# Kernel optimization log

Measured on AMD Instinct MI355X. Metric: run time of the kernel, lower is better.

## Reference

```python
import jax, jax.numpy as jnp
import numpy as np

N_NODES = 50000
N_EDGES = 800000
N_REL = 6
N_LAYERS = 8
D = 256
NUM_GRAPHS = 512


def setup_inputs() -> dict:
    key = jax.random.key(0)
    ks = jax.random.split(key, 24)
    s = lambda *sh: 1.0 / np.sqrt(sh[0])
    inp = {
        "x": jax.random.normal(ks[0], (N_NODES, 13), dtype=jnp.float32),
        "edge_index": jax.random.randint(ks[1], (2, N_EDGES), 0, N_NODES, dtype=jnp.int64),
        "edge_type": jax.random.randint(ks[2], (N_EDGES,), 0, N_REL, dtype=jnp.int64),
        "batch": jnp.sort(jax.random.randint(ks[3], (N_NODES,), 0, NUM_GRAPHS, dtype=jnp.int64)),
        "enc_W": jax.random.normal(ks[4], (13, D), dtype=jnp.float32) * s(13),
        "enc_b": jnp.zeros((D,), dtype=jnp.float32),
        "prelu_a": jnp.float32(0.25),
        "rel_W": jax.random.normal(ks[5], (N_LAYERS, N_REL, D, D), dtype=jnp.float32) * s(D),
        "root_W": jax.random.normal(ks[6], (N_LAYERS, D, D), dtype=jnp.float32) * s(D),
        "conv_b": jnp.zeros((N_LAYERS, D), dtype=jnp.float32),
        "gp_W1": jax.random.normal(ks[7], (D, D), dtype=jnp.float32) * s(D),
        "gp_b1": jnp.zeros((D,), dtype=jnp.float32),
        "gp_W2": jax.random.normal(ks[8], (D, D), dtype=jnp.float32) * s(D),
        "gp_b2": jnp.zeros((D,), dtype=jnp.float32),
        "fc_W1": jax.random.normal(ks[9], (D, 1024), dtype=jnp.float32) * s(D),
        "fc_b1": jnp.zeros((1024,), dtype=jnp.float32),
        "fc_W2": jax.random.normal(ks[10], (1024, 512), dtype=jnp.float32) * s(1024),
        "fc_b2": jnp.zeros((512,), dtype=jnp.float32),
        "out_W": jax.random.normal(ks[11], (512, 1), dtype=jnp.float32) * s(512),
        "out_b": jnp.zeros((1,), dtype=jnp.float32),
    }
    return inp


def reference(x, edge_index, edge_type, batch, enc_W, enc_b, prelu_a, rel_W, root_W,
              conv_b, gp_W1, gp_b1, gp_W2, gp_b2, fc_W1, fc_b1, fc_W2, fc_b2, out_W, out_b):
    src, dst = edge_index[0], edge_index[1]
    h = x @ enc_W + enc_b  # [N, D]
    for i in range(N_LAYERS):
        skip = h
        # per-relation transform for all nodes: [R, N, D]
        xW = jnp.einsum('nd,rde->rne', h, rel_W[i])
        msgs = xW[edge_type, src]  # [E, D] gather by (relation, source node)
        agg = jax.ops.segment_sum(msgs, dst, num_segments=N_NODES)
        h = agg + h @ root_W[i] + conv_b[i]
        h = h + skip
        h = jnp.where(h > 0, h, prelu_a * h)  # PReLU (shared scalar)
        norm = jnp.sqrt(jnp.sum(h * h, axis=1, keepdims=True))
        h = h / jnp.maximum(norm, 1e-12)  # F.normalize(p=2, dim=1)
    g = jax.nn.relu(h @ gp_W1 + gp_b1) @ gp_W2 + gp_b2
    pooled = jax.ops.segment_sum(g, batch, num_segments=NUM_GRAPHS)  # global_add_pool
    z = jax.nn.relu(pooled @ fc_W1 + fc_b1)  # dropout = identity at eval
    z = jax.nn.relu(z @ fc_W2 + fc_b2)
    return jax.nn.relu(z @ out_W + out_b)  # [NUM_GRAPHS, 1]
```

## Files before the change

### kernel.cpp

```cpp
#include <hip/hip_runtime.h>

#define N_NODES   50000
#define N_EDGES   800000
#define N_REL     6
#define N_LAYERS  8
#define DD        256
#define NUM_GRAPHS 512

#define NKEYS      (N_REL * N_NODES)
#define SCAN_T     256
#define SCAN_E     8
#define SCAN_CHUNK (SCAN_T * SCAN_E)
#define SCAN_NB    ((NKEYS + SCAN_CHUNK - 1) / SCAN_CHUNK)

typedef _Float16 h4 __attribute__((ext_vector_type(4)));
typedef _Float16 h8 __attribute__((ext_vector_type(8)));
typedef float    f4 __attribute__((ext_vector_type(4)));

__device__ __forceinline__ void atomAddF(float* p, float v) { unsafeAtomicAdd(p, v); }

__device__ __forceinline__ void load_lds16(const void* g, void* l) {
    __builtin_amdgcn_global_load_lds(
        (const __attribute__((address_space(1))) uint32_t*)g,
        (__attribute__((address_space(3))) uint32_t*)l, 16, 0, 0);
}

__global__ __launch_bounds__(256) void enc_kernel(const float* __restrict__ x,
                                                  const float* __restrict__ W,
                                                  const float* __restrict__ b,
                                                  _Float16* __restrict__ Hhi,
                                                  _Float16* __restrict__ Hlo) {
    int n = blockIdx.x;
    int d = threadIdx.x;
    float s = b[d];
#pragma unroll
    for (int k = 0; k < 13; ++k) s = fmaf(x[n * 13 + k], W[k * 256 + d], s);
    const _Float16 hi = (_Float16)s;
    Hhi[(size_t)n * DD + d] = hi;
    Hlo[(size_t)n * DD + d] = (_Float16)(s - (float)hi);
}

__global__ __launch_bounds__(256) void wsplit_rel_kernel(const float* __restrict__ relW,
                                                         const float* __restrict__ rootW,
                                                         _Float16* __restrict__ wthi,
                                                         _Float16* __restrict__ wtlo) {
    const size_t id = (size_t)blockIdx.x * 256 + threadIdx.x;
    if (id >= (size_t)N_LAYERS * 7 * 256 * 256) return;
    const int k = (int)(id & 255);
    const int n = (int)((id >> 8) & 255);
    const int g = (int)((id >> 16) % 7);
    const int L = (int)((id >> 16) / 7);
    float w = (g < 6)
        ? relW[(((size_t)L * 6 + g) * 256 + k) * 256 + n]
        : rootW[((size_t)L * 256 + k) * 256 + n];
    if (g == 6 && k == n) w += 1.0f;
    const _Float16 hi = (_Float16)w;
    const size_t o = ((size_t)L * 256 + n) * 1792 + (size_t)g * 256 + k;
    wthi[o] = hi;
    wtlo[o] = (_Float16)(w - (float)hi);
}

__global__ __launch_bounds__(256) void wsplit_tr_kernel(const float* __restrict__ W,
                                                        _Float16* __restrict__ whi,
                                                        _Float16* __restrict__ wlo,
                                                        int K, int N) {
    const size_t id = (size_t)blockIdx.x * 256 + threadIdx.x;
    if (id >= (size_t)K * N) return;
    const int k = (int)(id % K), n = (int)(id / K);
    const float w = W[(size_t)k * N + n];
    const _Float16 hi = (_Float16)w;
    whi[(size_t)n * K + k] = hi;
    wlo[(size_t)n * K + k] = (_Float16)(w - (float)hi);
}

__global__ __launch_bounds__(256) void fsplit_kernel(const float* __restrict__ S,
                                                     _Float16* __restrict__ hi,
                                                     _Float16* __restrict__ lo, int total) {
    const int id = blockIdx.x * 256 + threadIdx.x;
    if (id >= total) return;
    const float v = S[id];
    const _Float16 h = (_Float16)v;
    hi[id] = h;
    lo[id] = (_Float16)(v - (float)h);
}

template <int MODE>
__global__ __launch_bounds__(256, 2) void gemm_lds(
    const _Float16* __restrict__ Ahi, const _Float16* __restrict__ Alo,
    const _Float16* __restrict__ Hhi, const _Float16* __restrict__ Hlo,
    const _Float16* __restrict__ Bhi, const _Float16* __restrict__ Blo,
    int lda, int ldb, int ldc, int boff_agg, int boff_h, int K_agg, int K_tot,
    float* __restrict__ Cf, _Float16* __restrict__ Ohi, _Float16* __restrict__ Olo,
    const float* __restrict__ bias, const float* __restrict__ pa,
    float* __restrict__ ss4, int M) {
    __shared__ _Float16 smem[16384];
    const int lane = threadIdx.x & 63;
    const int wave = threadIdx.x >> 6;
    const int lm = lane & 15, lq = lane >> 4;
    const int wm = wave & 1, wn = wave >> 1;
    const int mb = blockIdx.x * 128;
    const int nb = blockIdx.y * 128;

    int uoff[2], arowg[2], browg[2], achk[2];
#pragma unroll
    for (int q = 0; q < 2; ++q) {
        const int u    = (q * 4 + wave) * 64 + lane;
        const int row  = u >> 2;
        const int slot = u & 3;
        const int c    = slot ^ ((row >> 1) & 3);
        uoff[q] = (q * 4 + wave) * 64;
        int rg = mb + row; if (rg >= M) rg = M - 1;
        arowg[q] = rg;
        browg[q] = nb + row;
        achk[q]  = c * 8;
    }

    f4 acc[4][4];
#pragma unroll
    for (int i = 0; i < 4; ++i)
#pragma unroll
        for (int j = 0; j < 4; ++j) acc[i][j] = (f4){0.f, 0.f, 0.f, 0.f};

    for (int k0 = 0; k0 < K_tot; k0 += 32) {
        const _Float16 *pAh, *pAl;
        int acol, bcol;
        if (k0 < K_agg) {
            const size_t pb = (size_t)(k0 >> 8) * (size_t)N_NODES * DD;
            pAh = Ahi + pb; pAl = Alo + pb;
            acol = k0 & 255;
            bcol = boff_agg + k0;
        } else {
            pAh = Hhi; pAl = Hlo;
            acol = k0 - K_agg;
            bcol = boff_h + (k0 - K_agg);
        }

        __syncthreads();
#pragma unroll
        for (int q = 0; q < 2; ++q) {
            const size_t ga = (size_t)arowg[q] * lda + acol + achk[q];
            const size_t gb = (size_t)browg[q] * ldb + bcol + achk[q];
            _Float16* lbase = smem + (size_t)uoff[q] * 8;
            load_lds16(pAh + ga, lbase);
            load_lds16(pAl + ga, lbase + 4096);
            load_lds16(Bhi + gb, lbase + 8192);
            load_lds16(Blo + gb, lbase + 12288);
        }
        __syncthreads();

        h8 ah[4], al[4], bh[4], bl[4];
#pragma unroll
        for (int i = 0; i < 4; ++i) {
            const int row  = wm * 64 + i * 16 + lm;
            const int slot = lq ^ ((row >> 1) & 3);
            const int o    = (row * 4 + slot) * 8;
            ah[i] = *(const h8*)(smem + o);
            al[i] = *(const h8*)(smem + 4096 + o);
        }
#pragma unroll
        for (int j = 0; j < 4; ++j) {
            const int n    = wn * 64 + j * 16 + lm;
            const int slot = lq ^ ((n >> 1) & 3);
            const int o    = (n * 4 + slot) * 8;
            bh[j] = *(const h8*)(smem + 8192 + o);
            bl[j] = *(const h8*)(smem + 12288 + o);
        }
#pragma unroll
        for (int i = 0; i < 4; ++i)
#pragma unroll
            for (int j = 0; j < 4; ++j) {
                acc[i][j] = __builtin_amdgcn_mfma_f32_16x16x32_f16(ah[i], bh[j], acc[i][j], 0, 0, 0);
                acc[i][j] = __builtin_amdgcn_mfma_f32_16x16x32_f16(ah[i], bl[j], acc[i][j], 0, 0, 0);
                acc[i][j] = __builtin_amdgcn_mfma_f32_16x16x32_f16(al[i], bh[j], acc[i][j], 0, 0, 0);
            }
    }

    if (MODE == 0) {
#pragma unroll
        for (int i = 0; i < 4; ++i)
#pragma unroll
            for (int r = 0; r < 4; ++r) {
                const int row = mb + wm * 64 + i * 16 + lq * 4 + r;
                if (row >= M) continue;
#pragma unroll
                for (int j = 0; j < 4; ++j) {
                    const int col = nb + wn * 64 + j * 16 + lm;
                    Cf[(size_t)row * ldc + col] = acc[i][j][r] + bias[col];
                }
            }
    } else if (MODE == 3) {
#pragma unroll
        for (int i = 0; i < 4; ++i)
#pragma unroll
            for (int r = 0; r < 4; ++r) {
                const int row = mb + wm * 64 + i * 16 + lq * 4 + r;
                if (row >= M) continue;
#pragma unroll
                for (int j = 0; j < 4; ++j) {
                    const int col = nb + wn * 64 + j * 16 + lm;
                    Cf[(size_t)row * ldc + col] += acc[i][j][r];
                }
            }
    } else if (MODE == 2) {
#pragma unroll
        for (int i = 0; i < 4; ++i)
#pragma unroll
            for (int r = 0; r < 4; ++r) {
                const int row = mb + wm * 64 + i * 16 + lq * 4 + r;
                if (row >= M) continue;
#pragma unroll
                for (int j = 0; j < 4; ++j) {
                    const int col = nb + wn * 64 + j * 16 + lm;
                    const float v = fmaxf(acc[i][j][r] + bias[col], 0.f);
                    const _Float16 hi = (_Float16)v;
                    const size_t idx = (size_t)row * ldc + col;
                    Ohi[idx] = hi;
                    Olo[idx] = (_Float16)(v - (float)hi);
                }
            }
    } else {
        const float a = pa[0];
#pragma unroll
        for (int i = 0; i < 4; ++i)
#pragma unroll
            for (int r = 0; r < 4; ++r) {
                const int row = mb + wm * 64 + i * 16 + lq * 4 + r;
                float rss = 0.f;
                if (row < M) {
#pragma unroll
                    for (int j = 0; j < 4; ++j) {
                        const int col = nb + wn * 64 + j * 16 + lm;
                        float v = acc[i][j][r] + Cf[(size_t)row * ldc + col];
                        v = v > 0.f ? v : a * v;
                        const _Float16 hi = (_Float16)v;
                        const size_t idx = (size_t)row * ldc + col;
                        Ohi[idx] = hi;
                        Olo[idx] = (_Float16)(v - (float)hi);
                        rss = fmaf(v, v, rss);
                    }
                }
                rss += __shfl_xor(rss, 1, 64);
                rss += __shfl_xor(rss, 2, 64);
                rss += __shfl_xor(rss, 4, 64);
                rss += __shfl_xor(rss, 8, 64);
                if (lm == 0 && row < M)
                    ss4[(size_t)row * 4 + blockIdx.y * 2 + wn] = rss;
            }
    }
}

__global__ __launch_bounds__(256) void norm_kernel(_Float16* __restrict__ Hhi,
                                                   _Float16* __restrict__ Hlo,
                                                   const float* __restrict__ ss4) {
    const int node = blockIdx.x * 4 + (threadIdx.x >> 6);
    const int lane = threadIdx.x & 63;
    if (node >= N_NODES) return;
    const float tot = ss4[node * 4 + 0] + ss4[node * 4 + 1] +
                      ss4[node * 4 + 2] + ss4[node * 4 + 3];
    const float inv = 1.0f / fmaxf(sqrtf(tot), 1e-12f);
    const size_t o = (size_t)node * DD + lane * 4;
    h4 vh = *(const h4*)(Hhi + o);
    h4 vl = *(const h4*)(Hlo + o);
    h4 oh, ol;
#pragma unroll
    for (int e = 0; e < 4; ++e) {
        const float v = ((float)vh[e] + (float)vl[e]) * inv;
        oh[e] = (_Float16)v;
        ol[e] = (_Float16)(v - (float)oh[e]);
    }
    *(h4*)(Hhi + o) = oh;
    *(h4*)(Hlo + o) = ol;
}

__global__ __launch_bounds__(256) void hist_kernel(const int* __restrict__ dst,
                                                   const int* __restrict__ etype,
                                                   int* __restrict__ cnt) {
    const int e = blockIdx.x * 256 + threadIdx.x;
    if (e >= N_EDGES) return;
    atomicAdd(&cnt[etype[e] * N_NODES + dst[e]], 1);
}

__global__ __launch_bounds__(SCAN_T) void scan1_kernel(const int* __restrict__ cnt,
                                                       int* __restrict__ off,
                                                       int* __restrict__ bsum) {
    __shared__ int sh[SCAN_T];
    const int b = blockIdx.x, t = threadIdx.x;
    const int base = b * SCAN_CHUNK + t * SCAN_E;
    int pre[SCAN_E];
    int s = 0;
#pragma unroll
    for (int i = 0; i < SCAN_E; ++i) {
        const int x = (base + i < NKEYS) ? cnt[base + i] : 0;
        pre[i] = s;
        s += x;
    }
    sh[t] = s;
    __syncthreads();
    for (int d = 1; d < SCAN_T; d <<= 1) {
        const int x = (t >= d) ? sh[t - d] : 0;
        __syncthreads();
        sh[t] += x;
        __syncthreads();
    }
    const int toff = (t == 0) ? 0 : sh[t - 1];
#pragma unroll
    for (int i = 0; i < SCAN_E; ++i)
        if (base + i < NKEYS) off[base + i] = toff + pre[i];
    if (t == SCAN_T - 1) bsum[b] = sh[SCAN_T - 1];
}

__global__ __launch_bounds__(SCAN_T) void scan2_kernel(int* __restrict__ bsum, int n) {
    __shared__ int sh[SCAN_T];
    const int t = threadIdx.x;
    const int base = t * SCAN_E;
    int pre[SCAN_E];
    int s = 0;
#pragma unroll
    for (int i = 0; i < SCAN_E; ++i) {
        const int x = (base + i < n) ? bsum[base + i] : 0;
        pre[i] = s;
        s += x;
    }
    sh[t] = s;
    __syncthreads();
    for (int d = 1; d < SCAN_T; d <<= 1) {
        const int x = (t >= d) ? sh[t - d] : 0;
        __syncthreads();
        sh[t] += x;
        __syncthreads();
    }
    const int toff = (t == 0) ? 0 : sh[t - 1];
#pragma unroll
    for (int i = 0; i < SCAN_E; ++i)
        if (base + i < n) bsum[base + i] = toff + pre[i];
}

__global__ __launch_bounds__(SCAN_T) void scan3_kernel(int* __restrict__ off,
                                                       const int* __restrict__ bsum) {
    const int b = blockIdx.x, t = threadIdx.x;
    const int add = bsum[b];
    const int base = b * SCAN_CHUNK + t * SCAN_E;
#pragma unroll
    for (int i = 0; i < SCAN_E; ++i)
        if (base + i < NKEYS) off[base + i] += add;
    if (b == 0 && t == 0) off[NKEYS] = N_EDGES;
}

__global__ __launch_bounds__(256) void csr_fill_kernel(const int* __restrict__ src,
                                                       const int* __restrict__ dst,
                                                       const int* __restrict__ etype,
                                                       int* __restrict__ cursor,
                                                       int* __restrict__ sorted_src) {
    const int e = blockIdx.x * 256 + threadIdx.x;
    if (e >= N_EDGES) return;
    const int key = etype[e] * N_NODES + dst[e];
    const int pos = atomicAdd(&cursor[key], 1);
    sorted_src[pos] = src[e];
}

__global__ __launch_bounds__(256) void agg2_kernel(const _Float16* __restrict__ Hhi,
                                                   const _Float16* __restrict__ Hlo,
                                                   const int* __restrict__ off,
                                                   const int* __restrict__ isrc,
                                                   _Float16* __restrict__ agghi,
                                                   _Float16* __restrict__ agglo, int rel0) {
    const int pair = blockIdx.x * 4 + (threadIdx.x >> 6);
    const int lane = threadIdx.x & 63;
    if (pair >= 2 * N_NODES) return;
    const int rl   = (pair >= N_NODES) ? 1 : 0;
    const int node = pair - rl * N_NODES;
    const int r    = rel0 + rl;
    const int s0 = off[r * N_NODES + node];
    const int s1 = off[r * N_NODES + node + 1];
    float a0 = 0.f, a1 = 0.f, a2 = 0.f, a3 = 0.f;
    for (int e = s0; e < s1; ++e) {
        const int s = isrc[e];
        const h4 vh = *(const h4*)(Hhi + (size_t)s * DD + lane * 4);
        const h4 vl = *(const h4*)(Hlo + (size_t)s * DD + lane * 4);
        a0 += (float)vh[0] + (float)vl[0];
        a1 += (float)vh[1] + (float)vl[1];
        a2 += (float)vh[2] + (float)vl[2];
        a3 += (float)vh[3] + (float)vl[3];
    }
    h4 oh, ol;
    oh[0] = (_Float16)a0; ol[0] = (_Float16)(a0 - (float)oh[0]);
    oh[1] = (_Float16)a1; ol[1] = (_Float16)(a1 - (float)oh[1]);
    oh[2] = (_Float16)a2; ol[2] = (_Float16)(a2 - (float)oh[2]);
    oh[3] = (_Float16)a3; ol[3] = (_Float16)(a3 - (float)oh[3]);
    const size_t o = ((size_t)rl * N_NODES + node) * DD + lane * 4;
    *(h4*)(agghi + o) = oh;
    *(h4*)(agglo + o) = ol;
}

__global__ __launch_bounds__(64) void pool_kernel(const float* __restrict__ g,
                                                  const int* __restrict__ batch,
                                                  float* __restrict__ pooled) {
    const int c     = threadIdx.x;
    const int start = blockIdx.x * 128;
    const int end   = min(start + 128, N_NODES);
    int cur = batch[start];
    float4 acc = {0.f, 0.f, 0.f, 0.f};
    for (int n = start; n < end; ++n) {
        const int bn = batch[n];
        if (bn != cur) {
            float* p = pooled + (size_t)cur * DD + c * 4;
            atomAddF(p + 0, acc.x); atomAddF(p + 1, acc.y);
            atomAddF(p + 2, acc.z); atomAddF(p + 3, acc.w);
            acc = {0.f, 0.f, 0.f, 0.f};
            cur = bn;
        }
        const float4 v = reinterpret_cast<const float4*>(g + (size_t)n * DD)[c];
        acc.x += v.x; acc.y += v.y; acc.z += v.z; acc.w += v.w;
    }
    float* p = pooled + (size_t)cur * DD + c * 4;
    atomAddF(p + 0, acc.x); atomAddF(p + 1, acc.y);
    atomAddF(p + 2, acc.z); atomAddF(p + 3, acc.w);
}

__global__ __launch_bounds__(64) void out_kernel(const _Float16* __restrict__ z2hi,
                                                 const _Float16* __restrict__ z2lo,
                                                 const float* __restrict__ W,
                                                 const float* __restrict__ b,
                                                 float* __restrict__ out) {
    const int g = blockIdx.x;
    const int t = threadIdx.x;
    float s = 0.f;
#pragma unroll
    for (int j = 0; j < 8; ++j) {
        const int idx = t + 64 * j;
        const float z = (float)z2hi[(size_t)g * 512 + idx] + (float)z2lo[(size_t)g * 512 + idx];
        s = fmaf(z, W[idx], s);
    }
#pragma unroll
    for (int off = 32; off; off >>= 1) s += __shfl_xor(s, off, 64);
    if (t == 0) {
        const float v = s + b[0];
        out[g] = v > 0.f ? v : 0.f;
    }
}

extern "C" void kernel_launch(void* const* d_in, const int* in_sizes, int n_in,
                              void* d_out, int out_size, void* d_ws, size_t ws_size,
                              hipStream_t stream) {
    const float* x       = (const float*)d_in[0];
    const int*   eidx    = (const int*)d_in[1];
    const int*   etype   = (const int*)d_in[2];
    const int*   batch   = (const int*)d_in[3];
    const float* enc_W   = (const float*)d_in[4];
    const float* enc_b   = (const float*)d_in[5];
    const float* prelu_a = (const float*)d_in[6];
    const float* rel_W   = (const float*)d_in[7];
    const float* root_W  = (const float*)d_in[8];
    const float* conv_b  = (const float*)d_in[9];
    const float* gp_W1   = (const float*)d_in[10];
    const float* gp_b1   = (const float*)d_in[11];
    const float* gp_W2   = (const float*)d_in[12];
    const float* gp_b2   = (const float*)d_in[13];
    const float* fc_W1   = (const float*)d_in[14];
    const float* fc_b1   = (const float*)d_in[15];
    const float* fc_W2   = (const float*)d_in[16];
    const float* fc_b2   = (const float*)d_in[17];
    const float* out_W   = (const float*)d_in[18];
    const float* out_b   = (const float*)d_in[19];
    float* out = (float*)d_out;

    uint8_t* wp = (uint8_t*)d_ws;
    auto alloc = [&](size_t bytes) {
        void* r = (void*)wp;
        wp += (bytes + 255) & ~(size_t)255;
        return r;
    };
    float*    base   = (float*)alloc((size_t)N_NODES * DD * 4);
    _Float16* Hhi    = (_Float16*)alloc((size_t)N_NODES * DD * 2);
    _Float16* Hlo    = (_Float16*)alloc((size_t)N_NODES * DD * 2);
    _Float16* agghi  = (_Float16*)alloc((size_t)2 * N_NODES * DD * 2);
    _Float16* agglo  = (_Float16*)alloc((size_t)2 * N_NODES * DD * 2);
    _Float16* wthi   = (_Float16*)alloc((size_t)N_LAYERS * 256 * 1792 * 2);
    _Float16* wtlo   = (_Float16*)alloc((size_t)N_LAYERS * 256 * 1792 * 2);
    _Float16* wtg1hi = (_Float16*)alloc((size_t)256 * 256 * 2);
    _Float16* wtg1lo = (_Float16*)alloc((size_t)256 * 256 * 2);
    _Float16* wtg2hi = (_Float16*)alloc((size_t)256 * 256 * 2);
    _Float16* wtg2lo = (_Float16*)alloc((size_t)256 * 256 * 2);
    _Float16* wtf1hi = (_Float16*)alloc((size_t)1024 * 256 * 2);
    _Float16* wtf1lo = (_Float16*)alloc((size_t)1024 * 256 * 2);
    _Float16* wtf2hi = (_Float16*)alloc((size_t)512 * 1024 * 2);
    _Float16* wtf2lo = (_Float16*)alloc((size_t)512 * 1024 * 2);
    float*    ss4    = (float*)alloc((size_t)N_NODES * 4 * 4);
    float*    pooled = (float*)alloc((size_t)NUM_GRAPHS * DD * 4);
    _Float16* phi    = (_Float16*)alloc((size_t)NUM_GRAPHS * DD * 2);
    _Float16* plo    = (_Float16*)alloc((size_t)NUM_GRAPHS * DD * 2);
    _Float16* z1hi   = (_Float16*)alloc((size_t)NUM_GRAPHS * 1024 * 2);
    _Float16* z1lo   = (_Float16*)alloc((size_t)NUM_GRAPHS * 1024 * 2);
    _Float16* z2hi   = (_Float16*)alloc((size_t)NUM_GRAPHS * 512 * 2);
    _Float16* z2lo   = (_Float16*)alloc((size_t)NUM_GRAPHS * 512 * 2);
    int*      ioff   = (int*)alloc((size_t)(NKEYS + 1) * 4);
    int*      icur   = (int*)alloc((size_t)NKEYS * 4);
    int*      ibsum  = (int*)alloc(256 * 4);
    int*      isrc   = (int*)alloc((size_t)N_EDGES * 4);

    const int* src = eidx;
    const int* dst = eidx + N_EDGES;

    const size_t wtot = (size_t)N_LAYERS * 7 * 256 * 256;
    wsplit_rel_kernel<<<(int)((wtot + 255) / 256), 256, 0, stream>>>(rel_W, root_W, wthi, wtlo);
    wsplit_tr_kernel<<<256, 256, 0, stream>>>(gp_W1, wtg1hi, wtg1lo, 256, 256);
    wsplit_tr_kernel<<<256, 256, 0, stream>>>(gp_W2, wtg2hi, wtg2lo, 256, 256);
    wsplit_tr_kernel<<<1024, 256, 0, stream>>>(fc_W1, wtf1hi, wtf1lo, 256, 1024);
    wsplit_tr_kernel<<<2048, 256, 0, stream>>>(fc_W2, wtf2hi, wtf2lo, 1024, 512);

    hipMemsetAsync(icur, 0, (size_t)NKEYS * sizeof(int), stream);
    const int eb = (N_EDGES + 255) / 256;
    hist_kernel<<<eb, 256, 0, stream>>>(dst, etype, icur);
    scan1_kernel<<<SCAN_NB, SCAN_T, 0, stream>>>(icur, ioff, ibsum);
    scan2_kernel<<<1, SCAN_T, 0, stream>>>(ibsum, SCAN_NB);
    scan3_kernel<<<SCAN_NB, SCAN_T, 0, stream>>>(ioff, ibsum);
    hipMemcpyAsync(icur, ioff, (size_t)NKEYS * sizeof(int), hipMemcpyDeviceToDevice, stream);
    csr_fill_kernel<<<eb, 256, 0, stream>>>(src, dst, etype, icur, isrc);

    enc_kernel<<<N_NODES, 256, 0, stream>>>(x, enc_W, enc_b, Hhi, Hlo);

    const dim3 gG((N_NODES + 127) / 128, 2);
    const int  nodeb = (N_NODES + 3) / 4;
    const int  aggb  = (2 * N_NODES + 3) / 4;

    for (int L = 0; L < N_LAYERS; ++L) {
        const _Float16* Bh = wthi + (size_t)L * 256 * 1792;
        const _Float16* Bl = wtlo + (size_t)L * 256 * 1792;
        agg2_kernel<<<aggb, 256, 0, stream>>>(Hhi, Hlo, ioff, isrc, agghi, agglo, 0);
        gemm_lds<0><<<gG, 256, 0, stream>>>(agghi, agglo, Hhi, Hlo, Bh, Bl,
                                            256, 1792, 256, 0, 1536, 512, 768,
                                            base, nullptr, nullptr,
                                            conv_b + L * DD, nullptr, nullptr, N_NODES);
        agg2_kernel<<<aggb, 256, 0, stream>>>(Hhi, Hlo, ioff, isrc, agghi, agglo, 2);
        gemm_lds<3><<<gG, 256, 0, stream>>>(agghi, agglo, Hhi, Hlo, Bh, Bl,
                                            256, 1792, 256, 512, 0, 512, 512,
                                            base, nullptr, nullptr,
                                            nullptr, nullptr, nullptr, N_NODES);
        agg2_kernel<<<aggb, 256, 0, stream>>>(Hhi, Hlo, ioff, isrc, agghi, agglo, 4);
        gemm_lds<1><<<gG, 256, 0, stream>>>(agghi, agglo, Hhi, Hlo, Bh, Bl,
                                            256, 1792, 256, 1024, 0, 512, 512,
                                            base, Hhi, Hlo,
                                            nullptr, prelu_a, ss4, N_NODES);
        norm_kernel<<<nodeb, 256, 0, stream>>>(Hhi, Hlo, ss4);
    }

    gemm_lds<2><<<gG, 256, 0, stream>>>(nullptr, nullptr, Hhi, Hlo, wtg1hi, wtg1lo,
                                        256, 256, 256, 0, 0, 0, 256,
                                        nullptr, agghi, agglo, gp_b1, nullptr, nullptr, N_NODES);
    gemm_lds<0><<<gG, 256, 0, stream>>>(agghi, agglo, nullptr, nullptr, wtg2hi, wtg2lo,
                                        256, 256, 256, 0, 0, 256, 256,
                                        base, nullptr, nullptr, gp_b2, nullptr, nullptr, N_NODES);

    hipMemsetAsync(pooled, 0, (size_t)NUM_GRAPHS * DD * sizeof(float), stream);
    pool_kernel<<<(N_NODES + 127) / 128, 64, 0, stream>>>(base, batch, pooled);
    fsplit_kernel<<<(NUM_GRAPHS * DD + 255) / 256, 256, 0, stream>>>(
        pooled, phi, plo, NUM_GRAPHS * DD);

    gemm_lds<2><<<dim3(4, 8), 256, 0, stream>>>(nullptr, nullptr, phi, plo, wtf1hi, wtf1lo,
                                                256, 256, 1024, 0, 0, 0, 256,
                                                nullptr, z1hi, z1lo, fc_b1, nullptr, nullptr,
                                                NUM_GRAPHS);
    gemm_lds<2><<<dim3(4, 4), 256, 0, stream>>>(nullptr, nullptr, z1hi, z1lo, wtf2hi, wtf2lo,
                                                1024, 1024, 512, 0, 0, 0, 1024,
                                                nullptr, z2hi, z2lo, fc_b2, nullptr, nullptr,
                                                NUM_GRAPHS);
    out_kernel<<<NUM_GRAPHS, 64, 0, stream>>>(z2hi, z2lo, out_W, out_b, out);
}
```

Baseline: 3.633 ms.

## Widen GEMM tile to full 256 columns, fuse L2 normalize, vectorize aggregation

The GEMM block now covers all 256 output columns (128x256 tile, 8 accumulator columns per wave), so each row's full norm can be computed in-block through shared memory. This lets the separate norm kernel and its ss4 buffer be removed, and the A tile no longer has to be reloaded for a second column block. The aggregation kernel now splits each wave into two halves that process alternating edges with 8-wide fp16 loads and combine the halves with a shuffle. In exchange the GEMM uses twice the accumulator registers and more LDS, which may lower occupancy, and the grid has half as many blocks.

```diff
diff --git a/kernel.cpp b/kernel.cpp
--- a/kernel.cpp
+++ b/kernel.cpp
@@ -91,35 +91,20 @@
     const _Float16* __restrict__ Bhi, const _Float16* __restrict__ Blo,
     int lda, int ldb, int ldc, int boff_agg, int boff_h, int K_agg, int K_tot,
     float* __restrict__ Cf, _Float16* __restrict__ Ohi, _Float16* __restrict__ Olo,
-    const float* __restrict__ bias, const float* __restrict__ pa,
-    float* __restrict__ ss4, int M) {
-    __shared__ _Float16 smem[16384];
+    const float* __restrict__ bias, const float* __restrict__ pa, int M) {
+    __shared__ _Float16 smem[24576];
     const int lane = threadIdx.x & 63;
     const int wave = threadIdx.x >> 6;
     const int lm = lane & 15, lq = lane >> 4;
     const int wm = wave & 1, wn = wave >> 1;
     const int mb = blockIdx.x * 128;
-    const int nb = blockIdx.y * 128;
-
-    int uoff[2], arowg[2], browg[2], achk[2];
-#pragma unroll
-    for (int q = 0; q < 2; ++q) {
-        const int u    = (q * 4 + wave) * 64 + lane;
-        const int row  = u >> 2;
-        const int slot = u & 3;
-        const int c    = slot ^ ((row >> 1) & 3);
-        uoff[q] = (q * 4 + wave) * 64;
-        int rg = mb + row; if (rg >= M) rg = M - 1;
-        arowg[q] = rg;
-        browg[q] = nb + row;
-        achk[q]  = c * 8;
-    }
-
-    f4 acc[4][4];
+    const int nb = blockIdx.y * 256;
+
+    f4 acc[4][8];
 #pragma unroll
     for (int i = 0; i < 4; ++i)
 #pragma unroll
-        for (int j = 0; j < 4; ++j) acc[i][j] = (f4){0.f, 0.f, 0.f, 0.f};
+        for (int j = 0; j < 8; ++j) acc[i][j] = (f4){0.f, 0.f, 0.f, 0.f};
 
     for (int k0 = 0; k0 < K_tot; k0 += 32) {
         const _Float16 *pAh, *pAl;
@@ -137,18 +122,28 @@
 
         __syncthreads();
 #pragma unroll
-        for (int q = 0; q < 2; ++q) {
-            const size_t ga = (size_t)arowg[q] * lda + acol + achk[q];
-            const size_t gb = (size_t)browg[q] * ldb + bcol + achk[q];
-            _Float16* lbase = smem + (size_t)uoff[q] * 8;
-            load_lds16(pAh + ga, lbase);
-            load_lds16(pAl + ga, lbase + 4096);
-            load_lds16(Bhi + gb, lbase + 8192);
-            load_lds16(Blo + gb, lbase + 12288);
-        }
-        __syncthreads();
-
-        h8 ah[4], al[4], bh[4], bl[4];
+        for (int q = 0; q < 12; ++q) {
+            const int ub = (q * 4 + wave) * 64;
+            const int u  = ub + lane;
+            const _Float16* gp;
+            size_t ga;
+            if (q < 4) {
+                const int v = u & 511, row = v >> 2, slot = v & 3;
+                const int c = slot ^ ((row >> 1) & 3);
+                int rg = mb + row; if (rg >= M) rg = M - 1;
+                gp = (q < 2) ? pAh : pAl;
+                ga = (size_t)rg * lda + acol + c * 8;
+            } else {
+                const int v = u & 1023, row = v >> 2, slot = v & 3;
+                const int c = slot ^ ((row >> 1) & 3);
+                gp = (q < 8) ? Bhi : Blo;
+                ga = (size_t)(nb + row) * ldb + bcol + c * 8;
+            }
+            load_lds16(gp + ga, smem + (size_t)ub * 8);
+        }
+        __syncthreads();
+
+        h8 ah[4], al[4], bh[8], bl[8];
 #pragma unroll
         for (int i = 0; i < 4; ++i) {
             const int row  = wm * 64 + i * 16 + lm;
@@ -158,17 +153,17 @@
             al[i] = *(const h8*)(smem + 4096 + o);
         }
 #pragma unroll
-        for (int j = 0; j < 4; ++j) {
-            const int n    = wn * 64 + j * 16 + lm;
+        for (int j = 0; j < 8; ++j) {
+            const int n    = wn * 128 + j * 16 + lm;
             const int slot = lq ^ ((n >> 1) & 3);
             const int o    = (n * 4 + slot) * 8;
             bh[j] = *(const h8*)(smem + 8192 + o);
-            bl[j] = *(const h8*)(smem + 12288 + o);
+            bl[j] = *(const h8*)(smem + 16384 + o);
         }
 #pragma unroll
         for (int i = 0; i < 4; ++i)
 #pragma unroll
-            for (int j = 0; j < 4; ++j) {
+            for (int j = 0; j < 8; ++j) {
                 acc[i][j] = __builtin_amdgcn_mfma_f32_16x16x32_f16(ah[i], bh[j], acc[i][j], 0, 0, 0);
                 acc[i][j] = __builtin_amdgcn_mfma_f32_16x16x32_f16(ah[i], bl[j], acc[i][j], 0, 0, 0);
                 acc[i][j] = __builtin_amdgcn_mfma_f32_16x16x32_f16(al[i], bh[j], acc[i][j], 0, 0, 0);
@@ -183,8 +178,8 @@
                 const int row = mb + wm * 64 + i * 16 + lq * 4 + r;
                 if (row >= M) continue;
 #pragma unroll
-                for (int j = 0; j < 4; ++j) {
-                    const int col = nb + wn * 64 + j * 16 + lm;
+                for (int j = 0; j < 8; ++j) {
+                    const int col = nb + wn * 128 + j * 16 + lm;
                     Cf[(size_t)row * ldc + col] = acc[i][j][r] + bias[col];
                 }
             }
@@ -196,8 +191,8 @@
                 const int row = mb + wm * 64 + i * 16 + lq * 4 + r;
                 if (row >= M) continue;
 #pragma unroll
-                for (int j = 0; j < 4; ++j) {
-                    const int col = nb + wn * 64 + j * 16 + lm;
+                for (int j = 0; j < 8; ++j) {
+                    const int col = nb + wn * 128 + j * 16 + lm;
                     Cf[(size_t)row * ldc + col] += acc[i][j][r];
                 }
             }
@@ -209,8 +204,8 @@
                 const int row = mb + wm * 64 + i * 16 + lq * 4 + r;
                 if (row >= M) continue;
 #pragma unroll
-                for (int j = 0; j < 4; ++j) {
-                    const int col = nb + wn * 64 + j * 16 + lm;
+                for (int j = 0; j < 8; ++j) {
+                    const int col = nb + wn * 128 + j * 16 + lm;
                     const float v = fmaxf(acc[i][j][r] + bias[col], 0.f);
                     const _Float16 hi = (_Float16)v;
                     const size_t idx = (size_t)row * ldc + col;
@@ -219,23 +214,23 @@
                 }
             }
     } else {
+        float* shf = (float*)smem;
         const float a = pa[0];
+        __syncthreads();
 #pragma unroll
         for (int i = 0; i < 4; ++i)
 #pragma unroll
             for (int r = 0; r < 4; ++r) {
-                const int row = mb + wm * 64 + i * 16 + lq * 4 + r;
+                const int rl  = i * 16 + lq * 4 + r;
+                const int row = mb + wm * 64 + rl;
                 float rss = 0.f;
                 if (row < M) {
 #pragma unroll
-                    for (int j = 0; j < 4; ++j) {
-                        const int col = nb + wn * 64 + j * 16 + lm;
+                    for (int j = 0; j < 8; ++j) {
+                        const int col = nb + wn * 128 + j * 16 + lm;
                         float v = acc[i][j][r] + Cf[(size_t)row * ldc + col];
                         v = v > 0.f ? v : a * v;
-                        const _Float16 hi = (_Float16)v;
-                        const size_t idx = (size_t)row * ldc + col;
-                        Ohi[idx] = hi;
-                        Olo[idx] = (_Float16)(v - (float)hi);
+                        acc[i][j][r] = v;
                         rss = fmaf(v, v, rss);
                     }
                 }
@@ -243,33 +238,29 @@
                 rss += __shfl_xor(rss, 2, 64);
                 rss += __shfl_xor(rss, 4, 64);
                 rss += __shfl_xor(rss, 8, 64);
-                if (lm == 0 && row < M)
-                    ss4[(size_t)row * 4 + blockIdx.y * 2 + wn] = rss;
-            }
-    }
-}
-
-__global__ __launch_bounds__(256) void norm_kernel(_Float16* __restrict__ Hhi,
-                                                   _Float16* __restrict__ Hlo,
-                                                   const float* __restrict__ ss4) {
-    const int node = blockIdx.x * 4 + (threadIdx.x >> 6);
-    const int lane = threadIdx.x & 63;
-    if (node >= N_NODES) return;
-    const float tot = ss4[node * 4 + 0] + ss4[node * 4 + 1] +
-                      ss4[node * 4 + 2] + ss4[node * 4 + 3];
-    const float inv = 1.0f / fmaxf(sqrtf(tot), 1e-12f);
-    const size_t o = (size_t)node * DD + lane * 4;
-    h4 vh = *(const h4*)(Hhi + o);
-    h4 vl = *(const h4*)(Hlo + o);
-    h4 oh, ol;
-#pragma unroll
-    for (int e = 0; e < 4; ++e) {
-        const float v = ((float)vh[e] + (float)vl[e]) * inv;
-        oh[e] = (_Float16)v;
-        ol[e] = (_Float16)(v - (float)oh[e]);
-    }
-    *(h4*)(Hhi + o) = oh;
-    *(h4*)(Hlo + o) = ol;
+                if (lm == 0 && row < M) shf[wave * 64 + rl] = rss;
+            }
+        __syncthreads();
+#pragma unroll
+        for (int i = 0; i < 4; ++i)
+#pragma unroll
+            for (int r = 0; r < 4; ++r) {
+                const int rl  = i * 16 + lq * 4 + r;
+                const int row = mb + wm * 64 + rl;
+                if (row >= M) continue;
+                const float tot = shf[wm * 64 + rl] + shf[(2 + wm) * 64 + rl];
+                const float inv = 1.0f / fmaxf(sqrtf(tot), 1e-12f);
+#pragma unroll
+                for (int j = 0; j < 8; ++j) {
+                    const int col = nb + wn * 128 + j * 16 + lm;
+                    const float v = acc[i][j][r] * inv;
+                    const _Float16 hi = (_Float16)v;
+                    const size_t idx = (size_t)row * ldc + col;
+                    Ohi[idx] = hi;
+                    Olo[idx] = (_Float16)(v - (float)hi);
+                }
+            }
+    }
 }
 
 __global__ __launch_bounds__(256) void hist_kernel(const int* __restrict__ dst,
@@ -366,30 +357,37 @@
                                                    _Float16* __restrict__ agglo, int rel0) {
     const int pair = blockIdx.x * 4 + (threadIdx.x >> 6);
     const int lane = threadIdx.x & 63;
+    const int half = lane >> 5, li = lane & 31;
     if (pair >= 2 * N_NODES) return;
     const int rl   = (pair >= N_NODES) ? 1 : 0;
     const int node = pair - rl * N_NODES;
     const int r    = rel0 + rl;
     const int s0 = off[r * N_NODES + node];
     const int s1 = off[r * N_NODES + node + 1];
-    float a0 = 0.f, a1 = 0.f, a2 = 0.f, a3 = 0.f;
-    for (int e = s0; e < s1; ++e) {
-        const int s = isrc[e];
-        const h4 vh = *(const h4*)(Hhi + (size_t)s * DD + lane * 4);
-        const h4 vl = *(const h4*)(Hlo + (size_t)s * DD + lane * 4);
-        a0 += (float)vh[0] + (float)vl[0];
-        a1 += (float)vh[1] + (float)vl[1];
-        a2 += (float)vh[2] + (float)vl[2];
-        a3 += (float)vh[3] + (float)vl[3];
-    }
-    h4 oh, ol;
-    oh[0] = (_Float16)a0; ol[0] = (_Float16)(a0 - (float)oh[0]);
-    oh[1] = (_Float16)a1; ol[1] = (_Float16)(a1 - (float)oh[1]);
-    oh[2] = (_Float16)a2; ol[2] = (_Float16)(a2 - (float)oh[2]);
-    oh[3] = (_Float16)a3; ol[3] = (_Float16)(a3 - (float)oh[3]);
-    const size_t o = ((size_t)rl * N_NODES + node) * DD + lane * 4;
-    *(h4*)(agghi + o) = oh;
-    *(h4*)(agglo + o) = ol;
+    float a[8] = {0.f, 0.f, 0.f, 0.f, 0.f, 0.f, 0.f, 0.f};
+    for (int e0 = s0; e0 < s1; e0 += 2) {
+        const int e = e0 + half;
+        if (e < s1) {
+            const int s = isrc[e];
+            const h8 vh = *(const h8*)(Hhi + (size_t)s * DD + li * 8);
+            const h8 vl = *(const h8*)(Hlo + (size_t)s * DD + li * 8);
+#pragma unroll
+            for (int k = 0; k < 8; ++k) a[k] += (float)vh[k] + (float)vl[k];
+        }
+    }
+#pragma unroll
+    for (int k = 0; k < 8; ++k) a[k] += __shfl_xor(a[k], 32, 64);
+    if (half == 0) {
+        h8 oh, ol;
+#pragma unroll
+        for (int k = 0; k < 8; ++k) {
+            oh[k] = (_Float16)a[k];
+            ol[k] = (_Float16)(a[k] - (float)oh[k]);
+        }
+        const size_t o = ((size_t)rl * N_NODES + node) * DD + li * 8;
+        *(h8*)(agghi + o) = oh;
+        *(h8*)(agglo + o) = ol;
+    }
 }
 
 __global__ __launch_bounds__(64) void pool_kernel(const float* __restrict__ g,
@@ -485,7 +483,6 @@
     _Float16* wtf1lo = (_Float16*)alloc((size_t)1024 * 256 * 2);
     _Float16* wtf2hi = (_Float16*)alloc((size_t)512 * 1024 * 2);
     _Float16* wtf2lo = (_Float16*)alloc((size_t)512 * 1024 * 2);
-    float*    ss4    = (float*)alloc((size_t)N_NODES * 4 * 4);
     float*    pooled = (float*)alloc((size_t)NUM_GRAPHS * DD * 4);
     _Float16* phi    = (_Float16*)alloc((size_t)NUM_GRAPHS * DD * 2);
     _Float16* plo    = (_Float16*)alloc((size_t)NUM_GRAPHS * DD * 2);
@@ -519,9 +516,8 @@
 
     enc_kernel<<<N_NODES, 256, 0, stream>>>(x, enc_W, enc_b, Hhi, Hlo);
 
-    const dim3 gG((N_NODES + 127) / 128, 2);
-    const int  nodeb = (N_NODES + 3) / 4;
-    const int  aggb  = (2 * N_NODES + 3) / 4;
+    const dim3 gG((N_NODES + 127) / 128, 1);
+    const int  aggb = (2 * N_NODES + 3) / 4;
 
     for (int L = 0; L < N_LAYERS; ++L) {
         const _Float16* Bh = wthi + (size_t)L * 256 * 1792;
@@ -530,39 +526,38 @@
         gemm_lds<0><<<gG, 256, 0, stream>>>(agghi, agglo, Hhi, Hlo, Bh, Bl,
                                             256, 1792, 256, 0, 1536, 512, 768,
                                             base, nullptr, nullptr,
-                                            conv_b + L * DD, nullptr, nullptr, N_NODES);
+                                            conv_b + L * DD, nullptr, N_NODES);
         agg2_kernel<<<aggb, 256, 0, stream>>>(Hhi, Hlo, ioff, isrc, agghi, agglo, 2);
         gemm_lds<3><<<gG, 256, 0, stream>>>(agghi, agglo, Hhi, Hlo, Bh, Bl,
                                             256, 1792, 256, 512, 0, 512, 512,
                                             base, nullptr, nullptr,
-                                            nullptr, nullptr, nullptr, N_NODES);
+                                            nullptr, nullptr, N_NODES);
         agg2_kernel<<<aggb, 256, 0, stream>>>(Hhi, Hlo, ioff, isrc, agghi, agglo, 4);
         gemm_lds<1><<<gG, 256, 0, stream>>>(agghi, agglo, Hhi, Hlo, Bh, Bl,
                                             256, 1792, 256, 1024, 0, 512, 512,
                                             base, Hhi, Hlo,
-                                            nullptr, prelu_a, ss4, N_NODES);
-        norm_kernel<<<nodeb, 256, 0, stream>>>(Hhi, Hlo, ss4);
+                                            nullptr, prelu_a, N_NODES);
     }
 
     gemm_lds<2><<<gG, 256, 0, stream>>>(nullptr, nullptr, Hhi, Hlo, wtg1hi, wtg1lo,
                                         256, 256, 256, 0, 0, 0, 256,
-                                        nullptr, agghi, agglo, gp_b1, nullptr, nullptr, N_NODES);
+                                        nullptr, agghi, agglo, gp_b1, nullptr, N_NODES);
     gemm_lds<0><<<gG, 256, 0, stream>>>(agghi, agglo, nullptr, nullptr, wtg2hi, wtg2lo,
                                         256, 256, 256, 0, 0, 256, 256,
-                                        base, nullptr, nullptr, gp_b2, nullptr, nullptr, N_NODES);
+                                        base, nullptr, nullptr, gp_b2, nullptr, N_NODES);
 
     hipMemsetAsync(pooled, 0, (size_t)NUM_GRAPHS * DD * sizeof(float), stream);
     pool_kernel<<<(N_NODES + 127) / 128, 64, 0, stream>>>(base, batch, pooled);
     fsplit_kernel<<<(NUM_GRAPHS * DD + 255) / 256, 256, 0, stream>>>(
         pooled, phi, plo, NUM_GRAPHS * DD);
 
-    gemm_lds<2><<<dim3(4, 8), 256, 0, stream>>>(nullptr, nullptr, phi, plo, wtf1hi, wtf1lo,
+    gemm_lds<2><<<dim3(4, 4), 256, 0, stream>>>(nullptr, nullptr, phi, plo, wtf1hi, wtf1lo,
                                                 256, 256, 1024, 0, 0, 0, 256,
-                                                nullptr, z1hi, z1lo, fc_b1, nullptr, nullptr,
+                                                nullptr, z1hi, z1lo, fc_b1, nullptr,
                                                 NUM_GRAPHS);
-    gemm_lds<2><<<dim3(4, 4), 256, 0, stream>>>(nullptr, nullptr, z1hi, z1lo, wtf2hi, wtf2lo,
+    gemm_lds<2><<<dim3(4, 2), 256, 0, stream>>>(nullptr, nullptr, z1hi, z1lo, wtf2hi, wtf2lo,
                                                 1024, 1024, 512, 0, 0, 0, 1024,
-                                                nullptr, z2hi, z2lo, fc_b2, nullptr, nullptr,
+                                                nullptr, z2hi, z2lo, fc_b2, nullptr,
                                                 NUM_GRAPHS);
     out_kernel<<<NUM_GRAPHS, 64, 0, stream>>>(z2hi, z2lo, out_W, out_b, out);
 }
```

Result: faster. 3.194 ms (-12.1%).
